# Optimization experiments

Hardware: AMD Instinct MI355X
Metric: run time of the kernel (lower is better)

The kernel has to match this reference:

```python
import jax, jax.numpy as jnp
import numpy as np

D = 1024
H = 16
HD = D // H  # per-head dim = 64
LQ = 2048
LK = 2048


def setup_inputs() -> dict:
    key = jax.random.key(0)
    ks = jax.random.split(key, 6)
    scale = 1.0 / np.sqrt(D)
    return {
        "input_embeddings": jax.random.normal(ks[0], (LQ, D), dtype=jnp.float32),
        "history_hidden": jax.random.normal(ks[1], (LK, D), dtype=jnp.float32),
        "W_q": jax.random.normal(ks[2], (D, D), dtype=jnp.float32) * scale,
        "W_k": jax.random.normal(ks[3], (D, D), dtype=jnp.float32) * scale,
        "W_v": jax.random.normal(ks[4], (D, D), dtype=jnp.float32) * scale,
        "W_o": jax.random.normal(ks[5], (D, D), dtype=jnp.float32) * scale,
    }


def reference(input_embeddings, history_hidden, W_q, W_k, W_v, W_o):
    # nn.Linear(bias=False): y = x @ W.T ; weights are [out, in]
    q = (input_embeddings @ W_q.T).reshape(LQ, H, HD)  # [Lq, H, hd]
    k = (history_hidden @ W_k.T).reshape(LK, H, HD)    # [Lk, H, hd]
    v = (history_hidden @ W_v.T).reshape(LK, H, HD)    # [Lk, H, hd]
    # per-head scaled dot-product attention, batched over heads
    scores = jnp.einsum("qhd,khd->hqk", q, k) / np.sqrt(HD).astype(np.float32)
    attn = jax.nn.softmax(scores, axis=-1)             # [H, Lq, Lk]
    ctx = jnp.einsum("hqk,khd->qhd", attn, v).reshape(LQ, D)
    # dropout p=0.0 -> identity
    return ctx @ W_o.T
```

## Files before the change

### kernel.cpp

```cpp
#include <hip/hip_runtime.h>

typedef __bf16 bf16x8 __attribute__((ext_vector_type(8)));
typedef __bf16 bf16x4 __attribute__((ext_vector_type(4)));
typedef float f32x4 __attribute__((ext_vector_type(4)));
typedef float f32x16 __attribute__((ext_vector_type(16)));
typedef unsigned short u16x4 __attribute__((ext_vector_type(4)));
typedef unsigned short u16x8 __attribute__((ext_vector_type(8)));

#define LQS 2048
#define LKS 2048
#define DMODEL 1024
#define NH 16
#define HDIM 64
#define NSPLIT 4
#define NT 8

#if __has_builtin(__builtin_amdgcn_exp2f)
#define EXP2(x) __builtin_amdgcn_exp2f(x)
#else
#define EXP2(x) exp2f(x)
#endif

#if __has_builtin(__builtin_amdgcn_mfma_f32_32x32x8bf16_1k)
#define HAS_K8 1
#else
#define HAS_K8 0
#endif

__device__ __forceinline__ unsigned short f2bf(float f) {
  union { float f; unsigned int u; } v; v.f = f;
  unsigned int r = v.u + 0x7FFFu + ((v.u >> 16) & 1u);
  return (unsigned short)(r >> 16);
}

__device__ __forceinline__ unsigned int pk2(float a, float b) {
  __bf16 lo = (__bf16)a, hi = (__bf16)b;
  unsigned short ul = __builtin_bit_cast(unsigned short, lo);
  unsigned short uh = __builtin_bit_cast(unsigned short, hi);
  return (unsigned)ul | ((unsigned)uh << 16);
}

#define ASYNC_CP16(gp, lp)                                                     \
  __builtin_amdgcn_global_load_lds(                                            \
      (const __attribute__((address_space(1))) unsigned int*)(gp),             \
      (__attribute__((address_space(3))) unsigned int*)(lp), 16, 0, 0)

struct CvtDesc { const float* src; unsigned short* dst; float scl; unsigned int nchunk; };
struct CvtBatch { CvtDesc d[6]; };

__global__ __launch_bounds__(256)
void cvt_all_k(CvtBatch cb) {
  unsigned int c = blockIdx.x * 256 + threadIdx.x;
#pragma unroll
  for (int s = 0; s < 6; ++s) {
    if (c < cb.d[s].nchunk) {
      const float* src = cb.d[s].src + (size_t)c * 8;
      float4 a = *(const float4*)(src);
      float4 b = *(const float4*)(src + 4);
      const float scl = cb.d[s].scl;
      u16x8 r;
      r[0] = f2bf(a.x * scl); r[1] = f2bf(a.y * scl);
      r[2] = f2bf(a.z * scl); r[3] = f2bf(a.w * scl);
      r[4] = f2bf(b.x * scl); r[5] = f2bf(b.y * scl);
      r[6] = f2bf(b.z * scl); r[7] = f2bf(b.w * scl);
      *(u16x8*)(cb.d[s].dst + (size_t)c * 8) = r;
      return;
    }
    c -= cb.d[s].nchunk;
  }
}

struct GemmDesc { const unsigned short* A; const unsigned short* B; void* C; int ldc; int transC; };
struct GemmBatch3 { GemmDesc d[3]; };

template<int BM, int BN, bool F32OUT>
__global__ __launch_bounds__(256)
void gemm_bt(GemmBatch3 gb, int K) {
  constexpr int MFR = BM / 32;
  constexpr int NFR = BN / 32;
  const GemmDesc g = gb.d[blockIdx.z];
  __shared__ __align__(16) unsigned short sA[2][BM * 32];
  __shared__ __align__(16) unsigned short sB[2][BN * 32];
  const int tid = threadIdx.x;
  const int w = tid >> 6, l = tid & 63;
  const int wr = w >> 1, wc = w & 1;
  const int lr = l & 15, lk = (l >> 4) * 8;
  const unsigned short* Ab = g.A + (size_t)(blockIdx.y * BM) * K;
  const unsigned short* Bb = g.B + (size_t)(blockIdx.x * BN) * K;
  const int srow = w * 16 + (l >> 2);
  const int scol = (l & 3) * 8;

  auto stage = [&](int buf, int k0) {
#pragma unroll
    for (int ia = 0; ia < BM / 64; ++ia)
      ASYNC_CP16(Ab + (size_t)(ia * 64 + srow) * K + k0 + scol,
                 sA[buf] + ia * 2048 + w * 512);
#pragma unroll
    for (int ib = 0; ib < BN / 64; ++ib)
      ASYNC_CP16(Bb + (size_t)(ib * 64 + srow) * K + k0 + scol,
                 sB[buf] + ib * 2048 + w * 512);
  };

  f32x4 acc[MFR][NFR] = {};
  stage(0, 0);
  __syncthreads();
  int cur = 0;
  for (int k0 = 0; k0 < K; k0 += 32) {
    if (k0 + 32 < K) stage(cur ^ 1, k0 + 32);
    bf16x8 af[MFR], bfr[NFR];
#pragma unroll
    for (int m = 0; m < MFR; ++m)
      af[m] = *(const bf16x8*)(sA[cur] + (wr * (BM / 2) + m * 16 + lr) * 32 + lk);
#pragma unroll
    for (int n = 0; n < NFR; ++n)
      bfr[n] = *(const bf16x8*)(sB[cur] + (wc * (BN / 2) + n * 16 + lr) * 32 + lk);
#pragma unroll
    for (int m = 0; m < MFR; ++m)
#pragma unroll
      for (int n = 0; n < NFR; ++n)
        acc[m][n] = __builtin_amdgcn_mfma_f32_16x16x32_bf16(af[m], bfr[n], acc[m][n], 0, 0, 0);
    __syncthreads();
    cur ^= 1;
  }
  const int r0 = blockIdx.y * BM + wr * (BM / 2) + (l >> 4) * 4;
  const int c0 = blockIdx.x * BN + wc * (BN / 2) + lr;
  if (g.transC) {
#pragma unroll
    for (int m = 0; m < MFR; ++m)
#pragma unroll
      for (int n = 0; n < NFR; ++n) {
        u16x4 v;
#pragma unroll
        for (int r = 0; r < 4; ++r) v[r] = f2bf(acc[m][n][r]);
        *(u16x4*)((unsigned short*)g.C + (size_t)(c0 + n * 16) * g.ldc + r0 + m * 16) = v;
      }
  } else {
#pragma unroll
    for (int m = 0; m < MFR; ++m)
#pragma unroll
      for (int n = 0; n < NFR; ++n)
#pragma unroll
        for (int r = 0; r < 4; ++r) {
          size_t idx = (size_t)(r0 + m * 16 + r) * g.ldc + c0 + n * 16;
          if (F32OUT) ((float*)g.C)[idx] = acc[m][n][r];
          else        ((unsigned short*)g.C)[idx] = f2bf(acc[m][n][r]);
        }
  }
}

__global__ __launch_bounds__(256)
void attn_k(const unsigned short* __restrict__ Q, const unsigned short* __restrict__ K,
            const unsigned short* __restrict__ Vt,
            __bf16* __restrict__ pacc, float* __restrict__ plsum) {
  __shared__ __align__(16) __bf16 sK[3][64 * 64];
  __shared__ __align__(16) __bf16 sV[3][64 * 64];
  const int b = blockIdx.x;
  const int xcd = b & 7, rr = b >> 3;
  const int qt = rr & 15, chi = rr >> 4;
  const int c = xcd + 8 * chi;
  const int h = c & 15, z = c >> 4;
  const int tid = threadIdx.x;
  const int w = tid >> 6, l = tid & 63;
  const int lq = l & 31;
  const int hi = l >> 5;
  const int qw0 = qt * 128 + w * 32;

  const int srow = l >> 3;
  const int scolb = (l & 7) * 16;

  bf16x8 qf[4];
#pragma unroll
  for (int t = 0; t < 4; ++t)
    qf[t] = *(const bf16x8*)(Q + (size_t)(qw0 + lq) * DMODEL + h * HDIM + t * 16 + hi * 8);

  f32x16 accO[2] = {};
#if HAS_K8
  f32x16 accsum = {};
  bf16x4 onesv;
#pragma unroll
  for (int j = 0; j < 4; ++j) onesv[j] = (__bf16)1.0f;
#else
  float lrun = 0.f;
#endif

  const int kt0 = z * (LKS / NSPLIT);

#define STAGE(B, KT)                                                           \
  do {                                                                         \
    _Pragma("unroll")                                                          \
    for (int i_ = 0; i_ < 2; ++i_) {                                           \
      const int row_ = (w * 2 + i_) * 8 + srow;                                \
      const int sc_ = scolb ^ ((row_ & 7) << 4);                               \
      ASYNC_CP16(K + (size_t)((KT) + row_) * DMODEL + h * HDIM + sc_ / 2,      \
                 (char*)(&sK[B][0]) + (w * 2 + i_) * 1024);                    \
      ASYNC_CP16(Vt + (size_t)(h * HDIM + row_) * LKS + (KT) + sc_ / 2,        \
                 (char*)(&sV[B][0]) + (w * 2 + i_) * 1024);                    \
    }                                                                          \
  } while (0)

  STAGE(0, kt0);
  STAGE(1, kt0 + 64);

#pragma unroll
  for (int t = 0; t < NT; ++t) {
    if (t >= 1) {
      __builtin_amdgcn_sched_barrier(0);
      __builtin_amdgcn_s_barrier();
    }
    if (t + 2 < NT) STAGE((t + 2) % 3, kt0 + (t + 2) * 64);
    if (t < NT - 2)       asm volatile("s_waitcnt vmcnt(8)" ::: "memory");
    else if (t == NT - 2) asm volatile("s_waitcnt vmcnt(4)" ::: "memory");
    else                  asm volatile("s_waitcnt vmcnt(0)" ::: "memory");
    __builtin_amdgcn_s_barrier();
    __builtin_amdgcn_sched_barrier(0);
    const int cur = t % 3;

    f32x16 sc[2] = {};
#pragma unroll
    for (int kb = 0; kb < 2; ++kb)
#pragma unroll
      for (int tt = 0; tt < 4; ++tt) {
        const int krow = kb * 32 + lq;
        const int cb = (tt * 32 + hi * 16) ^ ((krow & 7) << 4);
        bf16x8 kf = *(const bf16x8*)((const char*)(&sK[cur][0]) + krow * 128 + cb);
        sc[kb] = __builtin_amdgcn_mfma_f32_32x32x16_bf16(kf, qf[tt], sc[kb], 0, 0, 0);
      }
#pragma unroll
    for (int kb = 0; kb < 2; ++kb)
#pragma unroll
      for (int r = 0; r < 16; ++r)
        sc[kb][r] = EXP2(sc[kb][r]);
    unsigned int wd[2][8];
#pragma unroll
    for (int kb = 0; kb < 2; ++kb)
#pragma unroll
      for (int g = 0; g < 8; ++g)
        wd[kb][g] = pk2(sc[kb][2 * g], sc[kb][2 * g + 1]);

#if HAS_K8
    union W2 { unsigned int u[2]; bf16x4 v; };
#pragma unroll
    for (int g = 0; g < 8; ++g) {
      W2 a;
      a.u[0] = wd[g >> 2][2 * (g & 3)];
      a.u[1] = wd[g >> 2][2 * (g & 3) + 1];
#pragma unroll
      for (int db = 0; db < 2; ++db) {
        const int vrow = db * 32 + lq;
        const int cb = (16 * g + 8 * hi) ^ ((vrow & 7) << 4);
        bf16x4 bv = *(const bf16x4*)((const char*)(&sV[cur][0]) + vrow * 128 + cb);
        accO[db] = __builtin_amdgcn_mfma_f32_32x32x8bf16_1k(a.v, bv, accO[db], 0, 0, 0);
      }
      accsum = __builtin_amdgcn_mfma_f32_32x32x8bf16_1k(a.v, onesv, accsum, 0, 0, 0);
    }
#else
#pragma unroll
    for (int kb = 0; kb < 2; ++kb)
#pragma unroll
      for (int r = 0; r < 16; ++r) lrun += sc[kb][r];
    union PA { unsigned int u[4]; bf16x8 v; };
    PA pa[4];
#pragma unroll
    for (int ks = 0; ks < 4; ++ks) {
      const int kb = ks >> 1;
      const int g0 = (ks & 1) * 4;
      const unsigned int own0 = wd[kb][g0],     own1 = wd[kb][g0 + 1];
      const unsigned int oth0 = wd[kb][g0 + 2], oth1 = wd[kb][g0 + 3];
      const unsigned int off0 = hi ? own0 : oth0;
      const unsigned int off1 = hi ? own1 : oth1;
      const unsigned int rcv0 = (unsigned int)__shfl_xor((int)off0, 32);
      const unsigned int rcv1 = (unsigned int)__shfl_xor((int)off1, 32);
      pa[ks].u[0] = hi ? rcv0 : own0;
      pa[ks].u[1] = hi ? rcv1 : own1;
      pa[ks].u[2] = hi ? oth0 : rcv0;
      pa[ks].u[3] = hi ? oth1 : rcv1;
    }
#pragma unroll
    for (int db = 0; db < 2; ++db)
#pragma unroll
      for (int ks = 0; ks < 4; ++ks) {
        const int vrow = db * 32 + lq;
        const int cb = (ks * 32 + hi * 16) ^ ((vrow & 7) << 4);
        bf16x8 vf = *(const bf16x8*)((const char*)(&sV[cur][0]) + vrow * 128 + cb);
        accO[db] = __builtin_amdgcn_mfma_f32_32x32x16_bf16(pa[ks].v, vf, accO[db], 0, 0, 0);
      }
#endif
  }
#undef STAGE

#if HAS_K8
  if (lq == 0) {
#pragma unroll
    for (int r = 0; r < 16; ++r)
      plsum[((size_t)z * NH + h) * LQS + qw0 + (r & 3) + 8 * (r >> 2) + 4 * hi] = accsum[r];
  }
#else
  lrun += __shfl_xor(lrun, 32);
  if (hi == 0)
    plsum[((size_t)z * NH + h) * LQS + qw0 + lq] = lrun;
#endif
#pragma unroll
  for (int db = 0; db < 2; ++db)
#pragma unroll
    for (int r = 0; r < 16; ++r) {
      const int q = qw0 + (r & 3) + 8 * (r >> 2) + 4 * hi;
      pacc[(size_t)z * LQS * DMODEL + (size_t)q * DMODEL + h * HDIM + db * 32 + lq] =
          (__bf16)accO[db][r];
    }
}

__global__ __launch_bounds__(256)
void combine_k(const __bf16* pacc, const float* __restrict__ plsum, __bf16* ctx) {
  const size_t e = ((size_t)blockIdx.x * 256 + threadIdx.x) * 8;
  const int row = (int)(e >> 10), d0 = (int)(e & 1023), h = d0 >> 6;
  float lsum = 0.f;
  float acc[8] = {};
#pragma unroll
  for (int z = 0; z < NSPLIT; ++z) {
    lsum += plsum[((size_t)z * NH + h) * LQS + row];
    bf16x8 v = *(const bf16x8*)(pacc + (size_t)z * LQS * DMODEL + e);
#pragma unroll
    for (int j = 0; j < 8; ++j) acc[j] += (float)v[j];
  }
  float inv = 1.0f / lsum;
  bf16x8 r;
#pragma unroll
  for (int j = 0; j < 8; ++j) r[j] = (__bf16)(acc[j] * inv);
  *(bf16x8*)(ctx + e) = r;
}

extern "C" void kernel_launch(void* const* d_in, const int* in_sizes, int n_in,
                              void* d_out, int out_size, void* d_ws, size_t ws_size,
                              hipStream_t stream) {
  const float* x  = (const float*)d_in[0];
  const float* hh = (const float*)d_in[1];
  const float* wq = (const float*)d_in[2];
  const float* wk = (const float*)d_in[3];
  const float* wv = (const float*)d_in[4];
  const float* wo = (const float*)d_in[5];

  unsigned short* ws = (unsigned short*)d_ws;
  const size_t E2 = (size_t)LQS * DMODEL;
  const size_t E1 = (size_t)DMODEL * DMODEL;
  const size_t M = 1048576;
  unsigned short* xb  = ws;
  unsigned short* hb  = ws + 2 * M;
  unsigned short* wqb = ws + 4 * M;
  unsigned short* wkb = ws + 5 * M;
  unsigned short* wvb = ws + 6 * M;
  unsigned short* wob = ws + 8 * M;
  unsigned short* Qb  = ws + 9 * M;
  unsigned short* Kb  = ws + 11 * M;
  unsigned short* Vtb = ws + 13 * M;
  __bf16* pacc  = (__bf16*)ws;
  float*  plsum = (float*)(ws + 15 * M);
  unsigned short* cxb = ws;
  const float SCL = 0.125f * 1.4426950408889634f;

  CvtBatch cb;
  cb.d[0] = { x,  xb,  SCL, (unsigned)(E2 / 8) };
  cb.d[1] = { hh, hb,  1.f, (unsigned)(E2 / 8) };
  cb.d[2] = { wq, wqb, 1.f, (unsigned)(E1 / 8) };
  cb.d[3] = { wk, wkb, 1.f, (unsigned)(E1 / 8) };
  cb.d[4] = { wv, wvb, 1.f, (unsigned)(E1 / 8) };
  cb.d[5] = { wo, wob, 1.f, (unsigned)(E1 / 8) };
  cvt_all_k<<<dim3(4096), 256, 0, stream>>>(cb);

  GemmBatch3 qkv;
  qkv.d[0] = { xb, wqb, (void*)Qb,  DMODEL, 0 };
  qkv.d[1] = { hb, wkb, (void*)Kb,  DMODEL, 0 };
  qkv.d[2] = { hb, wvb, (void*)Vtb, LKS,    1 };
  gemm_bt<64, 128, false><<<dim3(DMODEL / 128, LQS / 64, 3), 256, 0, stream>>>(qkv, DMODEL);

  attn_k<<<dim3(16 * NH * NSPLIT), 256, 0, stream>>>(Qb, Kb, Vtb, pacc, plsum);

  combine_k<<<dim3((unsigned)(E2 / 2048)), 256, 0, stream>>>(pacc, plsum, (__bf16*)cxb);

  GemmBatch3 fin = {};
  fin.d[0] = { cxb, wob, d_out, DMODEL, 0 };
  gemm_bt<64, 64, true><<<dim3(DMODEL / 64, LQS / 64, 1), 256, 0, stream>>>(fin, DMODEL);
}
```

Before: 91.90 us.

## Fuse split-K attention combine into output projection GEMM A-loads; swizzle LDS

```diff
diff --git a/kernel.cpp b/kernel.cpp
--- a/kernel.cpp
+++ b/kernel.cpp
@@ -73,9 +73,9 @@
 struct GemmDesc { const unsigned short* A; const unsigned short* B; void* C; int ldc; int transC; };
 struct GemmBatch3 { GemmDesc d[3]; };
 
-template<int BM, int BN, bool F32OUT>
+template<int BM, int BN, bool F32OUT, bool FUSEA>
 __global__ __launch_bounds__(256)
-void gemm_bt(GemmBatch3 gb, int K) {
+void gemm_bt(GemmBatch3 gb, int K, const float* plsum) {
   constexpr int MFR = BM / 32;
   constexpr int NFR = BN / 32;
   const GemmDesc g = gb.d[blockIdx.z];
@@ -88,13 +88,40 @@
   const unsigned short* Ab = g.A + (size_t)(blockIdx.y * BM) * K;
   const unsigned short* Bb = g.B + (size_t)(blockIdx.x * BN) * K;
   const int srow = w * 16 + (l >> 2);
-  const int scol = (l & 3) * 8;
+  const int scol = (((l & 3) ^ (srow & 3)) * 8);
+  const int grow = blockIdx.y * BM + srow;
+  int curh = -1;
+  float inv = 0.f;
 
   auto stage = [&](int buf, int k0) {
-#pragma unroll
-    for (int ia = 0; ia < BM / 64; ++ia)
-      ASYNC_CP16(Ab + (size_t)(ia * 64 + srow) * K + k0 + scol,
-                 sA[buf] + ia * 2048 + w * 512);
+    if constexpr (FUSEA) {
+      const int hh = k0 >> 6;
+      if (hh != curh) {
+        curh = hh;
+        float s = 0.f;
+#pragma unroll
+        for (int z = 0; z < NSPLIT; ++z)
+          s += plsum[((size_t)z * NH + hh) * LQS + grow];
+        inv = 1.0f / s;
+      }
+      float a8[8] = {};
+#pragma unroll
+      for (int z = 0; z < NSPLIT; ++z) {
+        bf16x8 v = *(const bf16x8*)(g.A + (size_t)z * LQS * DMODEL +
+                                    (size_t)grow * K + k0 + scol);
+#pragma unroll
+        for (int j = 0; j < 8; ++j) a8[j] += (float)v[j];
+      }
+      u16x8 o;
+#pragma unroll
+      for (int j = 0; j < 8; ++j) o[j] = f2bf(a8[j] * inv);
+      *(u16x8*)(sA[buf] + w * 512 + l * 8) = o;
+    } else {
+#pragma unroll
+      for (int ia = 0; ia < BM / 64; ++ia)
+        ASYNC_CP16(Ab + (size_t)(ia * 64 + srow) * K + k0 + scol,
+                   sA[buf] + ia * 2048 + w * 512);
+    }
 #pragma unroll
     for (int ib = 0; ib < BN / 64; ++ib)
       ASYNC_CP16(Bb + (size_t)(ib * 64 + srow) * K + k0 + scol,
@@ -109,11 +136,15 @@
     if (k0 + 32 < K) stage(cur ^ 1, k0 + 32);
     bf16x8 af[MFR], bfr[NFR];
 #pragma unroll
-    for (int m = 0; m < MFR; ++m)
-      af[m] = *(const bf16x8*)(sA[cur] + (wr * (BM / 2) + m * 16 + lr) * 32 + lk);
-#pragma unroll
-    for (int n = 0; n < NFR; ++n)
-      bfr[n] = *(const bf16x8*)(sB[cur] + (wc * (BN / 2) + n * 16 + lr) * 32 + lk);
+    for (int m = 0; m < MFR; ++m) {
+      const int Ar = wr * (BM / 2) + m * 16 + lr;
+      af[m] = *(const bf16x8*)(sA[cur] + Ar * 32 + (((l >> 4) ^ (Ar & 3)) * 8));
+    }
+#pragma unroll
+    for (int n = 0; n < NFR; ++n) {
+      const int Br = wc * (BN / 2) + n * 16 + lr;
+      bfr[n] = *(const bf16x8*)(sB[cur] + Br * 32 + (((l >> 4) ^ (Br & 3)) * 8));
+    }
 #pragma unroll
     for (int m = 0; m < MFR; ++m)
 #pragma unroll
@@ -309,26 +340,6 @@
     }
 }
 
-__global__ __launch_bounds__(256)
-void combine_k(const __bf16* pacc, const float* __restrict__ plsum, __bf16* ctx) {
-  const size_t e = ((size_t)blockIdx.x * 256 + threadIdx.x) * 8;
-  const int row = (int)(e >> 10), d0 = (int)(e & 1023), h = d0 >> 6;
-  float lsum = 0.f;
-  float acc[8] = {};
-#pragma unroll
-  for (int z = 0; z < NSPLIT; ++z) {
-    lsum += plsum[((size_t)z * NH + h) * LQS + row];
-    bf16x8 v = *(const bf16x8*)(pacc + (size_t)z * LQS * DMODEL + e);
-#pragma unroll
-    for (int j = 0; j < 8; ++j) acc[j] += (float)v[j];
-  }
-  float inv = 1.0f / lsum;
-  bf16x8 r;
-#pragma unroll
-  for (int j = 0; j < 8; ++j) r[j] = (__bf16)(acc[j] * inv);
-  *(bf16x8*)(ctx + e) = r;
-}
-
 extern "C" void kernel_launch(void* const* d_in, const int* in_sizes, int n_in,
                               void* d_out, int out_size, void* d_ws, size_t ws_size,
                               hipStream_t stream) {
@@ -354,7 +365,6 @@
   unsigned short* Vtb = ws + 13 * M;
   __bf16* pacc  = (__bf16*)ws;
   float*  plsum = (float*)(ws + 15 * M);
-  unsigned short* cxb = ws;
   const float SCL = 0.125f * 1.4426950408889634f;
 
   CvtBatch cb;
@@ -370,13 +380,13 @@
   qkv.d[0] = { xb, wqb, (void*)Qb,  DMODEL, 0 };
   qkv.d[1] = { hb, wkb, (void*)Kb,  DMODEL, 0 };
   qkv.d[2] = { hb, wvb, (void*)Vtb, LKS,    1 };
-  gemm_bt<64, 128, false><<<dim3(DMODEL / 128, LQS / 64, 3), 256, 0, stream>>>(qkv, DMODEL);
+  gemm_bt<64, 128, false, false>
+      <<<dim3(DMODEL / 128, LQS / 64, 3), 256, 0, stream>>>(qkv, DMODEL, nullptr);
 
   attn_k<<<dim3(16 * NH * NSPLIT), 256, 0, stream>>>(Qb, Kb, Vtb, pacc, plsum);
 
-  combine_k<<<dim3((unsigned)(E2 / 2048)), 256, 0, stream>>>(pacc, plsum, (__bf16*)cxb);
-
   GemmBatch3 fin = {};
-  fin.d[0] = { cxb, wob, d_out, DMODEL, 0 };
-  gemm_bt<64, 64, true><<<dim3(DMODEL / 64, LQS / 64, 1), 256, 0, stream>>>(fin, DMODEL);
-}
+  fin.d[0] = { (const unsigned short*)pacc, wob, d_out, DMODEL, 0 };
+  gemm_bt<64, 64, true, true>
+      <<<dim3(DMODEL / 64, LQS / 64, 1), 256, 0, stream>>>(fin, DMODEL, plsum);
+}
```

After: 108.4 us. 18.0% more time.
